# Optimization experiments

Measured on AMD Instinct MI355X. Metric: run time of the kernel, lower is better.

Reference implementation:

```python
import jax, jax.numpy as jnp
import numpy as np

B, S, SV = 4, 2048, 50
QF = KF = VF = E = 1024
SCALE = np.float32(np.power(KF, 0.5))


def setup_inputs() -> dict:
    key = jax.random.key(0)
    ks = jax.random.split(key, 8)
    s = 0.02
    return {
        "Q": jax.random.normal(ks[0], (B, S, QF), dtype=jnp.float32),
        "K": jax.random.normal(ks[1], (B, S, KF), dtype=jnp.float32),
        "V": jax.random.normal(ks[2], (B, SV, VF), dtype=jnp.float32),
        # weights stored [in, out] so forward is x @ W (== torch Linear with weight.T)
        "W_Q": jax.random.normal(ks[3], (QF, E), dtype=jnp.float32) * s,
        "W_K": jax.random.normal(ks[4], (KF, E), dtype=jnp.float32) * s,
        "W_v": jax.random.normal(ks[5], (E, E), dtype=jnp.float32) * s,
        "W_vq": jax.random.normal(ks[6], (SV, E), dtype=jnp.float32) * s,
        "W_vk": jax.random.normal(ks[7], (SV, E), dtype=jnp.float32) * s,
    }


def reference(Q, K, V, W_Q, W_K, W_v, W_vq, W_vk):
    # mode == 'mode2', dropout=None (inference path)
    q = jnp.tanh(Q) @ W_Q          # [B,S,E]
    k = jnp.tanh(K) @ W_K          # [B,S,E]
    v = jnp.tanh(V) @ W_v          # [B,SV,E]

    qk = jnp.einsum('bse,bte->bst', q, k) / SCALE   # [B,S,S]
    vq = jnp.einsum('bse,bve->bsv', q, v) / SCALE   # [B,S,SV]
    vk = jnp.einsum('bse,bve->bsv', k, v) / SCALE   # [B,S,SV]

    f = jax.nn.softmax(qk, axis=-1)                 # [B,S,S]
    g = 1.0 - f

    q2 = jnp.einsum('bst,bte->bse', f, q) + vq @ W_vq
    k2 = jnp.einsum('bst,bte->bse', g, k) + vk @ W_vk

    Q_out = jnp.einsum('bst,bte->bse', f, q2)
    K_out = jnp.einsum('bst,bte->bse', g, k2)
    return (Q_out, K_out, f)
```

## Files before the change

kernel.cpp:

```cpp
#include <hip/hip_runtime.h>
#include <cstdint>
#include <cstddef>

typedef __bf16 bf16_t;
typedef __bf16 bf16x4 __attribute__((ext_vector_type(4)));
typedef __bf16 bf16x8 __attribute__((ext_vector_type(8)));
typedef float floatx4 __attribute__((ext_vector_type(4)));

#define B_ 4
#define S_ 2048
#define E_ 1024
#define SV_ 50
#define SVP_ 64
#define BSE_ ((long)B_ * S_ * E_)

__device__ __forceinline__ void async_copy16(const bf16_t* g, bf16_t* l) {
  __builtin_amdgcn_global_load_lds(
      (const __attribute__((address_space(1))) void*)g,
      (__attribute__((address_space(3))) void*)l, 16, 0, 0);
}

__global__ __launch_bounds__(256) void tanh2_k(const float* __restrict__ Q,
                                               const float* __restrict__ Kin,
                                               bf16_t* __restrict__ out) {
  long i4 = ((long)blockIdx.x * 256 + threadIdx.x) * 4;
  const long n = (long)B_ * S_ * E_;
  const float* src = (i4 < n) ? (Q + i4) : (Kin + (i4 - n));
  float4 x = *(const float4*)src;
  bf16x4 o;
  o[0] = (bf16_t)tanhf(x.x);
  o[1] = (bf16_t)tanhf(x.y);
  o[2] = (bf16_t)tanhf(x.z);
  o[3] = (bf16_t)tanhf(x.w);
  *(bf16x4*)&out[i4] = o;
}

__global__ __launch_bounds__(256) void tanh_vpad_k(const float* __restrict__ V,
                                                   bf16_t* __restrict__ out) {
  int i = blockIdx.x * 256 + threadIdx.x;
  int e = i & 1023, r = (i >> 10) & 63, b = i >> 16;
  float v = 0.f;
  if (r < SV_) v = tanhf(V[((long)(b * SV_ + r) << 10) + e]);
  out[i] = (bf16_t)v;
}

__global__ __launch_bounds__(256) void transp_cast3_k(const float* __restrict__ W0,
                                                      const float* __restrict__ W1,
                                                      const float* __restrict__ W2,
                                                      bf16_t* __restrict__ out,
                                                      int K, int N, int Kp) {
  __shared__ float tile[32][33];
  const float* W = (blockIdx.z == 0) ? W0 : (blockIdx.z == 1) ? W1 : W2;
  bf16_t* o = out + (long)blockIdx.z * N * Kp;
  int k0 = blockIdx.y * 32, n0 = blockIdx.x * 32;
  int tx = threadIdx.x, ty = threadIdx.y;
#pragma unroll
  for (int s2 = 0; s2 < 4; ++s2) {
    int kk = ty + s2 * 8;
    float v = 0.f;
    if (k0 + kk < K && n0 + tx < N) v = W[(long)(k0 + kk) * N + n0 + tx];
    tile[kk][tx] = v;
  }
  __syncthreads();
#pragma unroll
  for (int s2 = 0; s2 < 4; ++s2) {
    int nn = ty + s2 * 8;
    if (n0 + nn < N && k0 + tx < Kp)
      o[(long)(n0 + nn) * Kp + k0 + tx] = (bf16_t)tile[tx][nn];
  }
}

__global__ __launch_bounds__(256) void transp2_bf16_k(const bf16_t* __restrict__ in,
                                                      long selIn, long inRow,
                                                      long inBatch,
                                                      bf16_t* __restrict__ out,
                                                      long selOut, long outRow,
                                                      long outBatch,
                                                      float* __restrict__ csum) {
  __shared__ bf16_t tile[32][33];
  __shared__ float cs[8][32];
  int r0 = blockIdx.y * 32, c0 = blockIdx.x * 32;
  int tx = threadIdx.x, ty = threadIdx.y;
  int half = blockIdx.z & 1, bz = blockIdx.z >> 1;
  long ib = (long)bz * inBatch + (long)half * selIn;
  long ob = (long)bz * outBatch + (long)half * selOut;
  float ps = 0.f;
#pragma unroll
  for (int s2 = 0; s2 < 4; ++s2) {
    bf16_t v = in[ib + (long)(r0 + ty + s2 * 8) * inRow + c0 + tx];
    tile[ty + s2 * 8][tx] = v;
    ps += (float)v;
  }
  cs[ty][tx] = ps;
  __syncthreads();
#pragma unroll
  for (int s2 = 0; s2 < 4; ++s2)
    out[ob + (long)(c0 + ty + s2 * 8) * outRow + r0 + tx] = tile[tx][ty + s2 * 8];
  if (csum && half == 1 && ty == 0) {
    float s = 0.f;
#pragma unroll
    for (int c = 0; c < 8; ++c) s += cs[c][tx];
    atomicAdd(&csum[(long)bz * E_ + c0 + tx], s);
  }
}

__global__ __launch_bounds__(256) void softmax_row_k(bf16_t* __restrict__ fb,
                                                     float* __restrict__ Fout) {
  long off = ((long)blockIdx.y * S_ + blockIdx.x) * S_;
  int t = threadIdx.x;
  bf16x8 xb = *(const bf16x8*)&fb[off + 8 * t];
  float x[8];
#pragma unroll
  for (int i = 0; i < 8; ++i) x[i] = (float)xb[i];
  float mx = fmaxf(fmaxf(fmaxf(x[0], x[1]), fmaxf(x[2], x[3])),
                   fmaxf(fmaxf(x[4], x[5]), fmaxf(x[6], x[7])));
#pragma unroll
  for (int s = 32; s >= 1; s >>= 1) mx = fmaxf(mx, __shfl_xor(mx, s));
  __shared__ float red[4];
  int wv = t >> 6;
  if ((t & 63) == 0) red[wv] = mx;
  __syncthreads();
  mx = fmaxf(fmaxf(red[0], red[1]), fmaxf(red[2], red[3]));
  float e[8];
  float sum = 0.f;
#pragma unroll
  for (int i = 0; i < 8; ++i) {
    e[i] = __expf(x[i] - mx);
    sum += e[i];
  }
#pragma unroll
  for (int s = 32; s >= 1; s >>= 1) sum += __shfl_xor(sum, s);
  __shared__ float red2[4];
  if ((t & 63) == 0) red2[wv] = sum;
  __syncthreads();
  float inv = 1.0f / ((red2[0] + red2[1]) + (red2[2] + red2[3]));
  bf16x8 ob;
#pragma unroll
  for (int i = 0; i < 8; ++i) {
    e[i] *= inv;
    ob[i] = (bf16_t)e[i];
  }
  *(float4*)&Fout[off + 8 * t] = make_float4(e[0], e[1], e[2], e[3]);
  *(float4*)&Fout[off + 8 * t + 4] = make_float4(e[4], e[5], e[6], e[7]);
  *(bf16x8*)&fb[off + 8 * t] = ob;
}

__global__ __launch_bounds__(256) void gemm_vqk_k(const bf16_t* __restrict__ qkb,
                                                  const bf16_t* __restrict__ vb,
                                                  bf16_t* __restrict__ vqkf) {
  __shared__ __align__(16) bf16_t As[64 * 64];
  __shared__ __align__(16) bf16_t Bs[64 * 64];
  const int zz = blockIdx.z;
  const int sel = zz >> 2;
  const int b = zz & 3;
  const bf16_t* Ab = qkb + (long)sel * BSE_ + (long)b * S_ * E_;
  const bf16_t* Bb = vb + (long)b * SVP_ * E_;
  bf16_t* outB = vqkf + ((long)b * 2 + sel) * ((long)S_ * SVP_);
  const int t = threadIdx.x;
  const int lane = t & 63;
  const int wave = t >> 6;
  const int wm = (wave & 1) * 32;
  const int wn = (wave >> 1) * 32;
  const long rowBase = (long)blockIdx.y * 64;

  floatx4 acc[2][2];
#pragma unroll
  for (int i = 0; i < 2; ++i)
#pragma unroll
    for (int j = 0; j < 2; ++j) acc[i][j] = {0.f, 0.f, 0.f, 0.f};

  const int sr = t >> 3;
  const int sc = (t & 7) * 8;
  for (int k0 = 0; k0 < E_; k0 += 64) {
#pragma unroll
    for (int p = 0; p < 2; ++p) {
      int r = p * 32 + sr;
      *(uint4*)&As[r * 64 + sc] = *(const uint4*)&Ab[(rowBase + r) * E_ + k0 + sc];
      *(uint4*)&Bs[r * 64 + sc] = *(const uint4*)&Bb[(long)r * E_ + k0 + sc];
    }
    __syncthreads();
#pragma unroll
    for (int ks = 0; ks < 64; ks += 32) {
      const int fr = lane & 15;
      const int fk = ks + ((lane >> 4) << 3);
      bf16x8 a0 = *(const bf16x8*)&As[(wm + fr) * 64 + fk];
      bf16x8 a1 = *(const bf16x8*)&As[(wm + 16 + fr) * 64 + fk];
      bf16x8 b0 = *(const bf16x8*)&Bs[(wn + fr) * 64 + fk];
      bf16x8 b1 = *(const bf16x8*)&Bs[(wn + 16 + fr) * 64 + fk];
      acc[0][0] = __builtin_amdgcn_mfma_f32_16x16x32_bf16(a0, b0, acc[0][0], 0, 0, 0);
      acc[0][1] = __builtin_amdgcn_mfma_f32_16x16x32_bf16(a0, b1, acc[0][1], 0, 0, 0);
      acc[1][0] = __builtin_amdgcn_mfma_f32_16x16x32_bf16(a1, b0, acc[1][0], 0, 0, 0);
      acc[1][1] = __builtin_amdgcn_mfma_f32_16x16x32_bf16(a1, b1, acc[1][1], 0, 0, 0);
    }
    __syncthreads();
  }

  const int cr = lane & 15;
  const int rq = (lane >> 4) * 4;
  const float alpha = sel ? -1.f / 32.f : 1.f / 32.f;
#pragma unroll
  for (int i = 0; i < 2; ++i)
#pragma unroll
    for (int j = 0; j < 2; ++j)
#pragma unroll
      for (int r = 0; r < 4; ++r) {
        long row = rowBase + wm + i * 16 + rq + r;
        int col = wn + j * 16 + cr;
        outB[row * SVP_ + col] = (bf16_t)(alpha * acc[i][j][r]);
      }
}

__global__ __launch_bounds__(256, 4) void gemm_fused_k(
    const bf16_t* __restrict__ A1, long sA1,
    const bf16_t* __restrict__ B1, long sB1,
    int N, int K1,
    const bf16_t* __restrict__ A2q, const bf16_t* __restrict__ A2k, long sA2,
    const bf16_t* __restrict__ B2,
    float alpha, int negSplit, const float* __restrict__ colVec, long sV,
    float* __restrict__ outFa, bf16_t* __restrict__ outBa, int lda, long sOa,
    float* __restrict__ outFb, bf16_t* __restrict__ outBb, int ldb, long sOb,
    int capZ, int capM) {
  __shared__ __align__(16) bf16_t As[2 * 128 * 32];
  __shared__ __align__(16) bf16_t Bs[2 * 128 * 32];
  const int t = threadIdx.x;
  const int lane = t & 63;
  const int wave = t >> 6;
  const int wm = (wave & 1) * 64;
  const int wn = (wave >> 1) * 64;
  const long b = blockIdx.z;
  const long rowBase = (long)blockIdx.y * 128;
  const long colBase = (long)blockIdx.x * 128;
  if ((int)b >= capZ && rowBase >= capM) return;
  const bf16_t* Ab = A1 + b * sA1;
  const bf16_t* Bb = B1 + b * sB1;

  floatx4 acc[4][4];
#pragma unroll
  for (int i = 0; i < 4; ++i)
#pragma unroll
    for (int j = 0; j < 4; ++j) acc[i][j] = {0.f, 0.f, 0.f, 0.f};

  const int srow = lane >> 2;
  const int sch = lane & 3;
  const bf16_t* aG = Ab + (rowBase + wave * 16 + srow) * (long)K1 + sch * 8;
  const bf16_t* bG = Bb + (colBase + wave * 16 + srow) * (long)K1 + sch * 8;
  const long rStepA = (long)64 * K1;
  const int ldsW = (wave * 16) * 32;

  const int fr = lane & 15;
  const int hi = lane >> 4;
  int aoff[4], boff[4];
#pragma unroll
  for (int i = 0; i < 4; ++i) {
    aoff[i] = (wm + i * 16 + fr) * 32 + hi * 8;
    boff[i] = (wn + i * 16 + fr) * 32 + hi * 8;
  }

  const int nK1 = K1 >> 5;
  const int nt = nK1 + (A2q ? 2 : 0);

  auto stage = [&](int buf, int kt) {
    const int bo = buf * (128 * 32);
    if (kt < nK1) {
      const long k0 = (long)kt * 32;
#pragma unroll
      for (int p = 0; p < 2; ++p) {
        async_copy16(aG + p * rStepA + k0, &As[bo + p * 64 * 32 + ldsW]);
        async_copy16(bG + p * rStepA + k0, &Bs[bo + p * 64 * 32 + ldsW]);
      }
    } else {
      const int ts = kt - nK1;
      const bf16_t* A2 = (colBase >= negSplit) ? A2k : A2q;
      const bf16_t* A2b = A2 + b * sA2;
#pragma unroll
      for (int p = 0; p < 2; ++p) {
        long r = rowBase + p * 64 + wave * 16 + srow;
        long rc = colBase + p * 64 + wave * 16 + srow;
        async_copy16(A2b + r * 64 + ts * 32 + sch * 8, &As[bo + p * 64 * 32 + ldsW]);
        async_copy16(B2 + rc * 64 + ts * 32 + sch * 8, &Bs[bo + p * 64 * 32 + ldsW]);
      }
    }
  };

  stage(0, 0);
  if (nt > 1) stage(1, 1);

  for (int kt = 0; kt < nt; ++kt) {
    if (kt < nt - 1)
      asm volatile("s_waitcnt vmcnt(4)" ::: "memory");
    else
      asm volatile("s_waitcnt vmcnt(0)" ::: "memory");
    __builtin_amdgcn_s_barrier();
    __builtin_amdgcn_sched_barrier(0);
    const int bo = (kt & 1) * (128 * 32);
    __builtin_amdgcn_s_setprio(1);
    {
      bf16x8 af[4], bfr[4];
#pragma unroll
      for (int i = 0; i < 4; ++i) af[i] = *(const bf16x8*)&As[bo + aoff[i]];
#pragma unroll
      for (int i = 0; i < 4; ++i) bfr[i] = *(const bf16x8*)&Bs[bo + boff[i]];
#pragma unroll
      for (int i = 0; i < 4; ++i)
#pragma unroll
        for (int j = 0; j < 4; ++j)
          acc[i][j] =
              __builtin_amdgcn_mfma_f32_16x16x32_bf16(af[i], bfr[j], acc[i][j], 0, 0, 0);
    }
    __builtin_amdgcn_s_setprio(0);
    __builtin_amdgcn_sched_barrier(0);
    __builtin_amdgcn_s_barrier();
    __builtin_amdgcn_sched_barrier(0);
    if (kt + 2 < nt) stage(kt & 1, kt + 2);
  }

  const int cr = lane & 15;
  const int rq = hi * 4;
  const bool neg = (colBase >= negSplit);
  const float* cv = colVec ? (colVec + b * sV + (neg ? colBase - negSplit : colBase))
                           : nullptr;
  float* oF = neg ? outFb : outFa;
  bf16_t* oB = neg ? outBb : outBa;
  const int ld = neg ? ldb : lda;
  const long sO = neg ? sOb : sOa;
  const long cb0 = neg ? (long)(colBase - negSplit) : colBase;
#pragma unroll
  for (int i = 0; i < 4; ++i)
#pragma unroll
    for (int j = 0; j < 4; ++j)
#pragma unroll
      for (int r = 0; r < 4; ++r) {
        long row = rowBase + wm + i * 16 + rq + r;
        int c = wn + j * 16 + cr;
        float v = alpha * acc[i][j][r];
        if (neg) v = cv[c] - v;
        long o = b * sO + row * (long)ld + cb0 + c;
        if (oF) oF[o] = v;
        if (oB) oB[o] = (bf16_t)v;
      }
}

extern "C" void kernel_launch(void* const* d_in, const int* in_sizes, int n_in,
                              void* d_out, int out_size, void* d_ws, size_t ws_size,
                              hipStream_t stream) {
  const float* Q = (const float*)d_in[0];
  const float* Kin = (const float*)d_in[1];
  const float* V = (const float*)d_in[2];
  const float* W_Q = (const float*)d_in[3];
  const float* W_K = (const float*)d_in[4];
  const float* W_v = (const float*)d_in[5];
  const float* W_vq = (const float*)d_in[6];
  const float* W_vk = (const float*)d_in[7];

  float* Qout = (float*)d_out;
  float* Kout = Qout + (long)B_ * S_ * E_;
  float* Fout = Kout + (long)B_ * S_ * E_;

  char* w = (char*)d_ws;
  auto alloc = [&](size_t bytes) {
    char* p = w;
    w += (bytes + 255) & ~(size_t)255;
    return p;
  };
  const long BSE = BSE_;
  bf16_t* WQKt = (bf16_t*)alloc((size_t)2 * 2 * E_ * E_);
  bf16_t* WVt = (bf16_t*)alloc((size_t)2 * E_ * E_);
  bf16_t* Wv2T = (bf16_t*)alloc((size_t)2 * 2 * E_ * SVP_);
  bf16_t* QtKt = (bf16_t*)alloc((size_t)2 * 2 * BSE);
  bf16_t* Vt = (bf16_t*)alloc((size_t)2 * B_ * SVP_ * E_);
  bf16_t* qkb = (bf16_t*)alloc((size_t)2 * 2 * BSE);
  bf16_t* vb = (bf16_t*)alloc((size_t)2 * B_ * SVP_ * E_);
  bf16_t* qkT = (bf16_t*)alloc((size_t)2 * (long)B_ * 2 * E_ * S_);
  bf16_t* fb = (bf16_t*)alloc((size_t)2 * (long)B_ * S_ * S_);
  bf16_t* vqkf = (bf16_t*)alloc((size_t)2 * (long)B_ * 2 * S_ * SVP_);
  bf16_t* q2k2 = (bf16_t*)alloc((size_t)2 * (long)B_ * S_ * 2 * E_);
  bf16_t* q2k2T = (bf16_t*)alloc((size_t)2 * (long)B_ * 2 * E_ * S_);
  float* ck = (float*)alloc((size_t)4 * B_ * E_);
  float* ck2 = (float*)alloc((size_t)4 * B_ * E_);

  bf16_t* qb = qkb;
  bf16_t* kb = qkb + BSE;

  dim3 blk256(256);
  dim3 blk32x8(32, 8);

  hipMemsetAsync(ck, 0, (size_t)2 * 4 * B_ * E_, stream);

  transp_cast3_k<<<dim3(32, 32, 3), blk32x8, 0, stream>>>(W_Q, W_K, W_v, WQKt,
                                                          E_, E_, E_);
  transp_cast3_k<<<dim3(32, 2, 2), blk32x8, 0, stream>>>(W_vq, W_vk, W_vq, Wv2T,
                                                         SV_, E_, SVP_);

  tanh2_k<<<dim3((unsigned)(2 * BSE / 1024)), blk256, 0, stream>>>(Q, Kin, QtKt);
  tanh_vpad_k<<<dim3(B_ * SVP_ * E_ / 256), blk256, 0, stream>>>(V, Vt);

  gemm_fused_k<<<dim3(E_ / 128, B_ * S_ / 128, 3), blk256, 0, stream>>>(
      QtKt, BSE, WQKt, (long)E_ * E_, E_, E_,
      nullptr, nullptr, 0, nullptr, 1.f, E_, nullptr, 0,
      nullptr, qkb, E_, BSE, nullptr, nullptr, 0, 0,
      2, B_ * SVP_);

  transp2_bf16_k<<<dim3(E_ / 32, S_ / 32, 2 * B_), blk32x8, 0, stream>>>(
      qkb, BSE, E_, (long)S_ * E_, qkT, (long)E_ * S_, S_, (long)2 * E_ * S_, ck);

  gemm_fused_k<<<dim3(S_ / 128, S_ / 128, B_), blk256, 0, stream>>>(
      qb, (long)S_ * E_, kb, (long)S_ * E_, S_, E_,
      nullptr, nullptr, 0, nullptr, 1.f / 32.f, S_, nullptr, 0,
      nullptr, fb, S_, (long)S_ * S_, nullptr, nullptr, 0, 0,
      9999, 0);
  softmax_row_k<<<dim3(S_, B_), blk256, 0, stream>>>(fb, Fout);

  gemm_vqk_k<<<dim3(1, S_ / 64, 2 * B_), blk256, 0, stream>>>(qkb, vb, vqkf);

  gemm_fused_k<<<dim3(2 * E_ / 128, S_ / 128, B_), blk256, 0, stream>>>(
      fb, (long)S_ * S_, qkT, (long)2 * E_ * S_, 2 * E_, S_,
      vqkf, vqkf + (long)S_ * SVP_, (long)2 * S_ * SVP_, Wv2T,
      1.f, E_, ck, E_,
      nullptr, q2k2, 2 * E_, (long)S_ * 2 * E_,
      nullptr, q2k2 + E_, 2 * E_, (long)S_ * 2 * E_,
      9999, 0);

  transp2_bf16_k<<<dim3(E_ / 32, S_ / 32, 2 * B_), blk32x8, 0, stream>>>(
      q2k2, E_, 2 * E_, (long)S_ * 2 * E_, q2k2T, (long)E_ * S_, S_,
      (long)2 * E_ * S_, ck2);

  gemm_fused_k<<<dim3(2 * E_ / 128, S_ / 128, B_), blk256, 0, stream>>>(
      fb, (long)S_ * S_, q2k2T, (long)2 * E_ * S_, 2 * E_, S_,
      nullptr, nullptr, 0, nullptr,
      1.f, E_, ck2, E_,
      Qout, nullptr, E_, (long)S_ * E_,
      Kout, nullptr, E_, (long)S_ * E_,
      9999, 0);
}
```

Baseline: 579.6 us.

## Replace 128x128 GEMM with 256x256 tile, 8-wave, swizzled-LDS kernel

Swaps the shared GEMM kernel for one using 256x256 output tiles, 512 threads (8 waves), and a K-step of 64. The LDS layout is XOR-swizzled to avoid bank conflicts. The inner loop is split into four barrier-separated quadrants, with the next tile's async prefetch issued at the top of each iteration. The larger tiles raise arithmetic intensity and cut global traffic, at the cost of far more registers and LDS (128 KB per block) and fewer blocks, which can hurt occupancy and tail balance for the smaller GEMMs.

```diff
diff --git a/kernel.cpp b/kernel.cpp
--- a/kernel.cpp
+++ b/kernel.cpp
@@ -210,7 +210,7 @@
       }
 }
 
-__global__ __launch_bounds__(256, 4) void gemm_fused_k(
+__global__ __launch_bounds__(512, 2) void gemm256_k(
     const bf16_t* __restrict__ A1, long sA1,
     const bf16_t* __restrict__ B1, long sB1,
     int N, int K1,
@@ -220,98 +220,150 @@
     float* __restrict__ outFa, bf16_t* __restrict__ outBa, int lda, long sOa,
     float* __restrict__ outFb, bf16_t* __restrict__ outBb, int ldb, long sOb,
     int capZ, int capM) {
-  __shared__ __align__(16) bf16_t As[2 * 128 * 32];
-  __shared__ __align__(16) bf16_t Bs[2 * 128 * 32];
+  __shared__ __align__(16) bf16_t As[2 * 256 * 64];
+  __shared__ __align__(16) bf16_t Bs[2 * 256 * 64];
   const int t = threadIdx.x;
   const int lane = t & 63;
   const int wave = t >> 6;
-  const int wm = (wave & 1) * 64;
-  const int wn = (wave >> 1) * 64;
+  const int wr = wave >> 2;
+  const int wc = wave & 3;
   const long b = blockIdx.z;
-  const long rowBase = (long)blockIdx.y * 128;
-  const long colBase = (long)blockIdx.x * 128;
+  const long rowBase = (long)blockIdx.y * 256;
+  const long colBase = (long)blockIdx.x * 256;
   if ((int)b >= capZ && rowBase >= capM) return;
   const bf16_t* Ab = A1 + b * sA1;
   const bf16_t* Bb = B1 + b * sB1;
 
-  floatx4 acc[4][4];
-#pragma unroll
-  for (int i = 0; i < 4; ++i)
+  floatx4 acc[8][4];
+#pragma unroll
+  for (int i = 0; i < 8; ++i)
 #pragma unroll
     for (int j = 0; j < 4; ++j) acc[i][j] = {0.f, 0.f, 0.f, 0.f};
 
-  const int srow = lane >> 2;
-  const int sch = lane & 3;
-  const bf16_t* aG = Ab + (rowBase + wave * 16 + srow) * (long)K1 + sch * 8;
-  const bf16_t* bG = Bb + (colBase + wave * 16 + srow) * (long)K1 + sch * 8;
-  const long rStepA = (long)64 * K1;
-  const int ldsW = (wave * 16) * 32;
+  const int srow = t >> 3;
+  const int sch = (t & 7) ^ (srow & 7);
+  const bf16_t* aG = Ab + (rowBase + srow) * (long)K1 + sch * 8;
+  const bf16_t* bG = Bb + (colBase + srow) * (long)K1 + sch * 8;
+  const bf16_t* A2 = A2q ? ((colBase >= negSplit) ? A2k : A2q) : nullptr;
+  const bf16_t* a2G = A2 ? A2 + b * sA2 + (rowBase + srow) * 64 + sch * 8 : aG;
+  const bf16_t* b2G = A2 ? B2 + (colBase + srow) * 64 + sch * 8 : bG;
+  const int ldsW = (wave * 8) * 64;
 
   const int fr = lane & 15;
   const int hi = lane >> 4;
-  int aoff[4], boff[4];
-#pragma unroll
-  for (int i = 0; i < 4; ++i) {
-    aoff[i] = (wm + i * 16 + fr) * 32 + hi * 8;
-    boff[i] = (wn + i * 16 + fr) * 32 + hi * 8;
-  }
-
-  const int nK1 = K1 >> 5;
-  const int nt = nK1 + (A2q ? 2 : 0);
-
-  auto stage = [&](int buf, int kt) {
-    const int bo = buf * (128 * 32);
+  const int swz = (hi ^ (fr & 7)) * 8;
+  int aoff[8], boff[4];
+#pragma unroll
+  for (int i = 0; i < 8; ++i) aoff[i] = (wr * 128 + i * 16 + fr) * 64 + swz;
+#pragma unroll
+  for (int j = 0; j < 4; ++j) boff[j] = (wc * 64 + j * 16 + fr) * 64 + swz;
+
+  const int nK1 = K1 >> 6;
+  const int nt = nK1 + (A2q ? 1 : 0);
+
+  auto stageTile = [&](int buf, int kt) {
+    const int bo = buf * (256 * 64);
+    bf16_t* la = &As[bo + ldsW];
+    bf16_t* lb = &Bs[bo + ldsW];
     if (kt < nK1) {
-      const long k0 = (long)kt * 32;
-#pragma unroll
-      for (int p = 0; p < 2; ++p) {
-        async_copy16(aG + p * rStepA + k0, &As[bo + p * 64 * 32 + ldsW]);
-        async_copy16(bG + p * rStepA + k0, &Bs[bo + p * 64 * 32 + ldsW]);
+      const long k0 = (long)kt * 64;
+#pragma unroll
+      for (int h = 0; h < 4; ++h) {
+        async_copy16(aG + (long)(h * 64) * K1 + k0, la + h * 64 * 64);
+        async_copy16(bG + (long)(h * 64) * K1 + k0, lb + h * 64 * 64);
       }
     } else {
-      const int ts = kt - nK1;
-      const bf16_t* A2 = (colBase >= negSplit) ? A2k : A2q;
-      const bf16_t* A2b = A2 + b * sA2;
-#pragma unroll
-      for (int p = 0; p < 2; ++p) {
-        long r = rowBase + p * 64 + wave * 16 + srow;
-        long rc = colBase + p * 64 + wave * 16 + srow;
-        async_copy16(A2b + r * 64 + ts * 32 + sch * 8, &As[bo + p * 64 * 32 + ldsW]);
-        async_copy16(B2 + rc * 64 + ts * 32 + sch * 8, &Bs[bo + p * 64 * 32 + ldsW]);
+#pragma unroll
+      for (int h = 0; h < 4; ++h) {
+        async_copy16(a2G + h * 64 * 64, la + h * 64 * 64);
+        async_copy16(b2G + h * 64 * 64, lb + h * 64 * 64);
       }
     }
   };
 
-  stage(0, 0);
-  if (nt > 1) stage(1, 1);
+  stageTile(0, 0);
 
   for (int kt = 0; kt < nt; ++kt) {
-    if (kt < nt - 1)
-      asm volatile("s_waitcnt vmcnt(4)" ::: "memory");
-    else
+    const int bo = (kt & 1) * (256 * 64);
+    bf16x8 a0l[4], a0h[4], a1l[4], a1h[4], b0l[2], b0h[2], b1l[2], b1h[2];
+
+    if (kt + 1 < nt) {
+      stageTile((kt + 1) & 1, kt + 1);
+      asm volatile("s_waitcnt vmcnt(8)" ::: "memory");
+    } else {
       asm volatile("s_waitcnt vmcnt(0)" ::: "memory");
+    }
     __builtin_amdgcn_s_barrier();
     __builtin_amdgcn_sched_barrier(0);
-    const int bo = (kt & 1) * (128 * 32);
+#pragma unroll
+    for (int i = 0; i < 4; ++i) {
+      a0l[i] = *(const bf16x8*)&As[bo + aoff[i]];
+      a0h[i] = *(const bf16x8*)&As[bo + (aoff[i] ^ 32)];
+    }
+#pragma unroll
+    for (int j = 0; j < 2; ++j) {
+      b0l[j] = *(const bf16x8*)&Bs[bo + boff[j]];
+      b0h[j] = *(const bf16x8*)&Bs[bo + (boff[j] ^ 32)];
+    }
     __builtin_amdgcn_s_setprio(1);
-    {
-      bf16x8 af[4], bfr[4];
-#pragma unroll
-      for (int i = 0; i < 4; ++i) af[i] = *(const bf16x8*)&As[bo + aoff[i]];
-#pragma unroll
-      for (int i = 0; i < 4; ++i) bfr[i] = *(const bf16x8*)&Bs[bo + boff[i]];
-#pragma unroll
-      for (int i = 0; i < 4; ++i)
-#pragma unroll
-        for (int j = 0; j < 4; ++j)
-          acc[i][j] =
-              __builtin_amdgcn_mfma_f32_16x16x32_bf16(af[i], bfr[j], acc[i][j], 0, 0, 0);
-    }
+#pragma unroll
+    for (int i = 0; i < 4; ++i)
+#pragma unroll
+      for (int j = 0; j < 2; ++j) {
+        acc[i][j] = __builtin_amdgcn_mfma_f32_16x16x32_bf16(a0l[i], b0l[j], acc[i][j], 0, 0, 0);
+        acc[i][j] = __builtin_amdgcn_mfma_f32_16x16x32_bf16(a0h[i], b0h[j], acc[i][j], 0, 0, 0);
+      }
     __builtin_amdgcn_s_setprio(0);
     __builtin_amdgcn_sched_barrier(0);
+
     __builtin_amdgcn_s_barrier();
     __builtin_amdgcn_sched_barrier(0);
-    if (kt + 2 < nt) stage(kt & 1, kt + 2);
+#pragma unroll
+    for (int j = 0; j < 2; ++j) {
+      b1l[j] = *(const bf16x8*)&Bs[bo + boff[j + 2]];
+      b1h[j] = *(const bf16x8*)&Bs[bo + (boff[j + 2] ^ 32)];
+    }
+    __builtin_amdgcn_s_setprio(1);
+#pragma unroll
+    for (int i = 0; i < 4; ++i)
+#pragma unroll
+      for (int j = 0; j < 2; ++j) {
+        acc[i][j + 2] = __builtin_amdgcn_mfma_f32_16x16x32_bf16(a0l[i], b1l[j], acc[i][j + 2], 0, 0, 0);
+        acc[i][j + 2] = __builtin_amdgcn_mfma_f32_16x16x32_bf16(a0h[i], b1h[j], acc[i][j + 2], 0, 0, 0);
+      }
+    __builtin_amdgcn_s_setprio(0);
+    __builtin_amdgcn_sched_barrier(0);
+
+    __builtin_amdgcn_s_barrier();
+    __builtin_amdgcn_sched_barrier(0);
+#pragma unroll
+    for (int i = 0; i < 4; ++i) {
+      a1l[i] = *(const bf16x8*)&As[bo + aoff[i + 4]];
+      a1h[i] = *(const bf16x8*)&As[bo + (aoff[i + 4] ^ 32)];
+    }
+    __builtin_amdgcn_s_setprio(1);
+#pragma unroll
+    for (int i = 0; i < 4; ++i)
+#pragma unroll
+      for (int j = 0; j < 2; ++j) {
+        acc[i + 4][j + 2] = __builtin_amdgcn_mfma_f32_16x16x32_bf16(a1l[i], b1l[j], acc[i + 4][j + 2], 0, 0, 0);
+        acc[i + 4][j + 2] = __builtin_amdgcn_mfma_f32_16x16x32_bf16(a1h[i], b1h[j], acc[i + 4][j + 2], 0, 0, 0);
+      }
+    __builtin_amdgcn_s_setprio(0);
+    __builtin_amdgcn_sched_barrier(0);
+
+    __builtin_amdgcn_s_barrier();
+    __builtin_amdgcn_sched_barrier(0);
+    __builtin_amdgcn_s_setprio(1);
+#pragma unroll
+    for (int i = 0; i < 4; ++i)
+#pragma unroll
+      for (int j = 0; j < 2; ++j) {
+        acc[i + 4][j] = __builtin_amdgcn_mfma_f32_16x16x32_bf16(a1l[i], b0l[j], acc[i + 4][j], 0, 0, 0);
+        acc[i + 4][j] = __builtin_amdgcn_mfma_f32_16x16x32_bf16(a1h[i], b0h[j], acc[i + 4][j], 0, 0, 0);
+      }
+    __builtin_amdgcn_s_setprio(0);
+    __builtin_amdgcn_sched_barrier(0);
   }
 
   const int cr = lane & 15;
@@ -325,13 +377,13 @@
   const long sO = neg ? sOb : sOa;
   const long cb0 = neg ? (long)(colBase - negSplit) : colBase;
 #pragma unroll
-  for (int i = 0; i < 4; ++i)
+  for (int i = 0; i < 8; ++i)
 #pragma unroll
     for (int j = 0; j < 4; ++j)
 #pragma unroll
       for (int r = 0; r < 4; ++r) {
-        long row = rowBase + wm + i * 16 + rq + r;
-        int c = wn + j * 16 + cr;
+        long row = rowBase + wr * 128 + i * 16 + rq + r;
+        int c = wc * 64 + j * 16 + cr;
         float v = alpha * acc[i][j][r];
         if (neg) v = cv[c] - v;
         long o = b * sO + row * (long)ld + cb0 + c;
@@ -382,6 +434,7 @@
   bf16_t* kb = qkb + BSE;
 
   dim3 blk256(256);
+  dim3 blk512(512);
   dim3 blk32x8(32, 8);
 
   hipMemsetAsync(ck, 0, (size_t)2 * 4 * B_ * E_, stream);
@@ -394,7 +447,7 @@
   tanh2_k<<<dim3((unsigned)(2 * BSE / 1024)), blk256, 0, stream>>>(Q, Kin, QtKt);
   tanh_vpad_k<<<dim3(B_ * SVP_ * E_ / 256), blk256, 0, stream>>>(V, Vt);
 
-  gemm_fused_k<<<dim3(E_ / 128, B_ * S_ / 128, 3), blk256, 0, stream>>>(
+  gemm256_k<<<dim3(E_ / 256, B_ * S_ / 256, 3), blk512, 0, stream>>>(
       QtKt, BSE, WQKt, (long)E_ * E_, E_, E_,
       nullptr, nullptr, 0, nullptr, 1.f, E_, nullptr, 0,
       nullptr, qkb, E_, BSE, nullptr, nullptr, 0, 0,
@@ -403,7 +456,7 @@
   transp2_bf16_k<<<dim3(E_ / 32, S_ / 32, 2 * B_), blk32x8, 0, stream>>>(
       qkb, BSE, E_, (long)S_ * E_, qkT, (long)E_ * S_, S_, (long)2 * E_ * S_, ck);
 
-  gemm_fused_k<<<dim3(S_ / 128, S_ / 128, B_), blk256, 0, stream>>>(
+  gemm256_k<<<dim3(S_ / 256, S_ / 256, B_), blk512, 0, stream>>>(
       qb, (long)S_ * E_, kb, (long)S_ * E_, S_, E_,
       nullptr, nullptr, 0, nullptr, 1.f / 32.f, S_, nullptr, 0,
       nullptr, fb, S_, (long)S_ * S_, nullptr, nullptr, 0, 0,
@@ -412,7 +465,7 @@
 
   gemm_vqk_k<<<dim3(1, S_ / 64, 2 * B_), blk256, 0, stream>>>(qkb, vb, vqkf);
 
-  gemm_fused_k<<<dim3(2 * E_ / 128, S_ / 128, B_), blk256, 0, stream>>>(
+  gemm256_k<<<dim3(2 * E_ / 256, S_ / 256, B_), blk512, 0, stream>>>(
       fb, (long)S_ * S_, qkT, (long)2 * E_ * S_, 2 * E_, S_,
       vqkf, vqkf + (long)S_ * SVP_, (long)2 * S_ * SVP_, Wv2T,
       1.f, E_, ck, E_,
@@ -424,7 +477,7 @@
       q2k2, E_, 2 * E_, (long)S_ * 2 * E_, q2k2T, (long)E_ * S_, S_,
       (long)2 * E_ * S_, ck2);
 
-  gemm_fused_k<<<dim3(2 * E_ / 128, S_ / 128, B_), blk256, 0, stream>>>(
+  gemm256_k<<<dim3(2 * E_ / 256, S_ / 256, B_), blk512, 0, stream>>>(
       fb, (long)S_ * S_, q2k2T, (long)2 * E_ * S_, 2 * E_, S_,
       nullptr, nullptr, 0, nullptr,
       1.f, E_, ck2, E_,
```

Result: no change. 572.9 us (-1.2%).
